# Kernel tuning notes

Measured on AMD Instinct MI355X. Metric: run time of the kernel, lower is better.

The kernel has to match this reference:

```python
import math
import jax
import jax.numpy as jnp
import numpy as np

B = 2; Hrv = 16; Wrv = 1024; Crv = 64; Cb = 128; Cout = 128
D = 128; K = 5; NH = 8; NP = 4; DH = D // NH
Hbev = 220; Wbev = 220
RMAX = 55.0; XMIN = -55.0; XMAX = 55.0; YMIN = -55.0; YMAX = 55.0
EDGE_GAIN = 4.0; KLW = 1e-4

ELEV = np.array([-30.67, -29.33, -28.0, -26.66, -25.33, -24.0, -22.67, -21.33, -20.0, -18.67, -17.33, -16.0, -14.67, -13.33, -12.0, -10.67, -9.33, -8.0, -6.66, -5.33, -4.0, -2.67, -1.33, 0.0, 1.33, 2.67, 4.0, 5.33, 6.67, 8.0, 9.33, 10.67], dtype=np.float32)


def _buffers():
    groups = ELEV[::-1].reshape(Hrv, 32 // Hrv)
    steps = np.deg2rad(groups.max(1) - groups.min(1)).astype(np.float32)
    # torch Tensor.repeat == tile (faithful to original, even though rows end up interleaved)
    elev_steps = np.tile(steps, Wrv).reshape(Hrv, Wrv)
    means = np.deg2rad(groups.mean(1)).astype(np.float32)
    elevation = np.repeat(means, Wrv).reshape(Hrv, Wrv)  # numpy repeat == elementwise
    az_line = np.linspace(-np.pi, np.pi, Wrv + 1, dtype=np.float64)[:-1]
    az_step = float(az_line[1] - az_line[0])
    az_line = (az_line + az_step / 2).astype(np.float32)
    azimuth = np.broadcast_to(az_line[None, :], (Hrv, Wrv)).astype(np.float32).copy()
    offsets = np.linspace(-0.6, 0.6, K).astype(np.float32)
    u_vec = np.stack([np.cos(elevation) * np.cos(azimuth), np.cos(elevation) * np.sin(azimuth), np.sin(elevation)], 0).astype(np.float32)
    return (jnp.asarray(elev_steps), jnp.asarray(elevation), jnp.asarray(azimuth), az_step, jnp.asarray(offsets), jnp.asarray(u_vec))


def conv1x1(x, w, b):
    return jnp.einsum('bchw,oc->bohw', x, w) + b[None, :, None, None]


def groupnorm(x, g, gamma, beta, eps=1e-5):
    b_, c, h, w = x.shape
    xr = x.reshape(b_, g, c // g, h, w)
    m = xr.mean(axis=(2, 3, 4), keepdims=True)
    v = xr.var(axis=(2, 3, 4), keepdims=True)
    xn = ((xr - m) * jax.lax.rsqrt(v + eps)).reshape(b_, c, h, w)
    return xn * gamma[None, :, None, None] + beta[None, :, None, None]


def bilinear_sample(v_t, loc, H, W):
    # v_t: [B,NH,H*W,DH]; loc: [B,Nq,NH,NP,2] in [0,1]; grid_sample align_corners=False, zeros pad
    x = loc[..., 0] * W - 0.5
    y = loc[..., 1] * H - 0.5
    x0 = jnp.floor(x); y0 = jnp.floor(y)
    wx = x - x0; wy = y - y0
    x0i = x0.astype(jnp.int32); y0i = y0.astype(jnp.int32)
    b_, n_, nh_, p_ = x.shape

    def gather(xi, yi):
        valid = (xi >= 0) & (xi < W) & (yi >= 0) & (yi < H)
        idx = jnp.clip(yi, 0, H - 1) * W + jnp.clip(xi, 0, W - 1)
        idx_t = idx.transpose(0, 2, 1, 3).reshape(b_, nh_, n_ * p_)
        g = jnp.take_along_axis(v_t, idx_t[..., None], axis=2).reshape(b_, nh_, n_, p_, -1)
        return g * valid.transpose(0, 2, 1, 3)[..., None]

    wxt = wx.transpose(0, 2, 1, 3)[..., None]
    wyt = wy.transpose(0, 2, 1, 3)[..., None]
    g = gather(x0i, y0i) * (1 - wxt) * (1 - wyt)
    g = g + gather(x0i + 1, y0i) * wxt * (1 - wyt)
    g = g + gather(x0i, y0i + 1) * (1 - wxt) * wyt
    g = g + gather(x0i + 1, y0i + 1) * wxt * wyt
    return g  # [B,NH,Nq,NP,DH]


def setup_inputs():
    key = jax.random.key(0)
    ks = jax.random.split(key, 20)
    def rn(k, shape, s=0.02):
        return jax.random.normal(k, shape, jnp.float32) * s
    inp = {}
    inp['x_rv'] = jax.random.normal(ks[0], (B, Hrv, Wrv, Crv), jnp.float32)
    inp['bev'] = jax.random.normal(ks[1], (B, Cb, Hbev, Wbev), jnp.float32)
    inp['lidar2ego_mat'] = jnp.eye(4, dtype=jnp.float32)[None] + 0.01 * jax.random.normal(ks[2], (1, 4, 4), jnp.float32)
    inp['w_q'] = rn(ks[3], (D, Crv)); inp['b_q'] = jnp.zeros((D,), jnp.float32)
    inp['w_v'] = rn(ks[4], (D, Cb)); inp['b_v'] = jnp.zeros((D,), jnp.float32)
    inp['w_o'] = rn(ks[5], (Cout, D)); inp['b_o'] = jnp.zeros((Cout,), jnp.float32)
    inp['qs_w1'] = rn(ks[6], (D, D + 6)); inp['qs_b1'] = jnp.zeros((D,), jnp.float32)
    inp['qs_w2'] = rn(ks[7], (D, D)); inp['qs_b2'] = jnp.zeros((D,), jnp.float32)
    inp['rh_w1'] = rn(ks[8], (128, Crv + 3)); inp['rh_b1'] = jnp.zeros((128,), jnp.float32)
    inp['rh_g1'] = jnp.ones((128,), jnp.float32); inp['rh_bt1'] = jnp.zeros((128,), jnp.float32)
    inp['rh_w2'] = rn(ks[9], (64, 128, 3, 3))
    inp['rh_g2'] = jnp.ones((64,), jnp.float32); inp['rh_bt2'] = jnp.zeros((64,), jnp.float32)
    inp['rh_w3'] = rn(ks[10], (4, 64)); inp['rh_b3'] = jnp.zeros((4,), jnp.float32)
    inp['off_w'] = rn(ks[11], (NH * K * NP * 2, D)); inp['off_b'] = rn(ks[12], (NH * K * NP * 2,), 0.5)
    inp['aw_w'] = rn(ks[13], (NH * K * NP, D)); inp['aw_b'] = jnp.zeros((NH * K * NP,), jnp.float32)
    inp['val_w'] = rn(ks[14], (D, D)); inp['val_b'] = jnp.zeros((D,), jnp.float32)
    inp['out_w'] = rn(ks[15], (D, D)); inp['out_b'] = jnp.zeros((D,), jnp.float32)
    return inp


def reference(x_rv, bev, lidar2ego_mat, w_q, b_q, w_v, b_v, w_o, b_o, qs_w1, qs_b1, qs_w2, qs_b2, rh_w1, rh_b1, rh_g1, rh_bt1, rh_w2, rh_g2, rh_bt2, rh_w3, rh_b3, off_w, off_b, aw_w, aw_b, val_w, val_b, out_w, out_b):
    elev_steps, elevation, azimuth, az_step, offsets, u_vec = _buffers()
    x = jnp.transpose(x_rv, (0, 3, 1, 2))  # [B,Crv,Hrv,Wrv]
    Q0 = conv1x1(x, w_q, b_q)
    Vmap = conv1x1(bev, w_v, b_v)
    range_in = jnp.concatenate([x, jnp.broadcast_to(u_vec[None], (B, 3, Hrv, Wrv))], axis=1)
    h = jax.nn.gelu(groupnorm(conv1x1(range_in, rh_w1, rh_b1), 8, rh_g1, rh_bt1), approximate=False)
    hp = jnp.pad(h, ((0, 0), (0, 0), (1, 1), (1, 1)), mode='wrap')  # circular padding
    h = jax.lax.conv_general_dilated(hp, rh_w2, (1, 1), 'VALID', dimension_numbers=('NCHW', 'OIHW', 'NCHW'))
    h = jax.nn.gelu(groupnorm(h, 8, rh_g2, rh_bt2), approximate=False)
    head = conv1x1(h, rh_w3, rh_b3)  # [B,4,Hrv,Wrv]
    mu = jax.nn.sigmoid(head[:, 0:1]) * RMAX
    sd = jax.nn.softplus(head[:, 1:2]) + 1e-3
    se = jax.nn.sigmoid(head[:, 2:3]) * elev_steps + 1e-3
    sa = jax.nn.sigmoid(head[:, 3:4]) * az_step + 1e-3
    depth = mu[:, 0][..., None] + sd[:, 0][..., None] * offsets  # [B,Hrv,Wrv,K]
    elevs = elevation[None, :, :, None] + se[:, 0][..., None] * offsets
    azs = azimuth[None, :, :, None] + sa[:, 0][..., None] * offsets
    ce = jnp.cos(elevs)
    x_l = depth * ce * jnp.cos(azs)
    y_l = depth * ce * jnp.sin(azs)
    z_l = depth * jnp.sin(elevs)
    NK = Hrv * Wrv * K
    p = jnp.stack([x_l.reshape(B, NK), y_l.reshape(B, NK), z_l.reshape(B, NK), jnp.ones((B, NK), x_l.dtype)], axis=-1)
    p_ego = jnp.matmul(p, lidar2ego_mat)  # [B,NK,4]
    rx = jax.nn.sigmoid(EDGE_GAIN * ((p_ego[..., 0] - XMIN) / (XMAX - XMIN) - 0.5))
    ry = jax.nn.sigmoid(EDGE_GAIN * ((p_ego[..., 1] - YMIN) / (YMAX - YMIN) - 0.5))
    ref = jnp.stack([rx, ry], axis=-1).reshape(B, Hrv * Wrv, K, 2)
    sig_feat = jnp.concatenate([sd, se, sa, 1.0 / (sd + 1e-6), 1.0 / (se + 1e-6), 1.0 / (sa + 1e-6)], axis=1)
    Q = conv1x1(jax.nn.gelu(conv1x1(jnp.concatenate([Q0, sig_feat], axis=1), qs_w1, qs_b1), approximate=False), qs_w2, qs_b2)
    query = jnp.transpose(Q, (0, 2, 3, 1)).reshape(B, Hrv * Wrv, D)
    value = jnp.transpose(Vmap.reshape(B, D, Hbev * Wbev), (0, 2, 1))  # [B,HW,D]
    # MSDA -- all K levels share the same BEV value map (value was repeat(1,K,1))
    v = (value @ val_w.T + val_b).reshape(B, Hbev * Wbev, NH, DH)
    v_t = jnp.transpose(v, (0, 2, 1, 3))  # [B,NH,HW,DH]
    Nq = Hrv * Wrv
    smp_off = (query @ off_w.T + off_b).reshape(B, Nq, NH, K, NP, 2)
    attn = jax.nn.softmax((query @ aw_w.T + aw_b).reshape(B, Nq, NH, K * NP), axis=-1).reshape(B, Nq, NH, K, NP)
    norm = jnp.array([Wbev, Hbev], jnp.float32)
    loc = ref[:, :, None, :, None, :] + smp_off / norm  # [B,Nq,NH,K,NP,2]
    out = jnp.zeros((B, Nq, NH, DH), jnp.float32)
    for l in range(K):
        smp = bilinear_sample(v_t, loc[:, :, :, l], Hbev, Wbev)
        out = out + jnp.einsum('bhnpd,bnhp->bnhd', smp, attn[:, :, :, l])
    y_msda = out.reshape(B, Nq, D) @ out_w.T + out_b + query  # mmcv identity residual
    y = jnp.transpose(y_msda.reshape(B, Hrv, Wrv, D), (0, 3, 1, 2))
    y = conv1x1(y, w_o, b_o)
    mu_norm = mu / RMAX
    sr = jnp.maximum(sd, 1e-6)
    saz = sa / az_step
    sel = se / elev_steps
    L_kl = 0.5 * (mu_norm ** 2 + sr ** 2 - jnp.log(sr ** 2) - 1.0) \
         + 0.5 * (saz ** 2 - jnp.log(saz ** 2) - 1.0) \
         + 0.5 * (sel ** 2 - jnp.log(sel ** 2) - 1.0)
    kl = KLW * L_kl.mean()
    y = y.reshape(B, Hrv, Wrv, -1)  # faithful to torch .view on NCHW (no permute)
    return (y, kl)
```

## Files before the change

### kernel.cpp

```cpp
#include <hip/hip_runtime.h>
#include <math.h>

#define HRV 16
#define WRV 1024
#define NPIX 16384
#define NBEV 48400
#define BSZ 2

typedef __attribute__((ext_vector_type(8))) short short8;
typedef __attribute__((ext_vector_type(4))) float f32x4;

struct RVConsts {
  float steps[16];
  float means[16];
  float az_step_f;
  float pad_;
  double step_d;
  double az0;
  double az_half;
};

__device__ __forceinline__ float geluf(float x) {
  return 0.5f * x * (1.0f + erff(x * 0.70710678118654752440f));
}
__device__ __forceinline__ float sigmoidf_(float x) {
  return 1.0f / (1.0f + expf(-x));
}
__device__ __forceinline__ float softplusf_(float x) {
  return fmaxf(x, 0.0f) + log1pf(expf(-fabsf(x)));
}
__device__ __forceinline__ float azimf(int w, double step_d, double az0, double az_half) {
  double az = (double)w * step_d + az0;
  az += az_half;
  return (float)az;
}
__device__ __forceinline__ unsigned short f2bf(float f) {
  unsigned int u = __builtin_bit_cast(unsigned int, f);
  u = u + 0x7FFFu + ((u >> 16) & 1u);
  return (unsigned short)(u >> 16);
}
__device__ __forceinline__ float bf2f(unsigned short h) {
  unsigned int u = ((unsigned int)h) << 16;
  return __builtin_bit_cast(float, u);
}

__global__ __launch_bounds__(256) void k_rh1_q0(
    const float* __restrict__ x_rv,
    const unsigned short* __restrict__ rhW1p, const float* __restrict__ rh_b1,
    const unsigned short* __restrict__ wqp, const float* __restrict__ b_q,
    float* __restrict__ t1, unsigned short* __restrict__ q0,
    float* __restrict__ sums1, RVConsts C) {
  __shared__ unsigned short xin[64][104];
  __shared__ float wred[4][8][2];
  int b = blockIdx.y;
  int n0 = blockIdx.x * 64;
  int tid = threadIdx.x;
  const float* src = x_rv + ((size_t)b * NPIX + n0) * 64;
  for (int i = tid; i < 1024; i += 256) {
    int p = i >> 4, c = (i & 15) * 4;
    float4 v4 = *(const float4*)(src + p * 64 + c);
    xin[p][c] = f2bf(v4.x);
    xin[p][c + 1] = f2bf(v4.y);
    xin[p][c + 2] = f2bf(v4.z);
    xin[p][c + 3] = f2bf(v4.w);
  }
  if (tid < 64) {
    int n = n0 + tid;
    int h = n >> 10, w = n & 1023;
    float E = C.means[h];
    float A = azimf(w, C.step_d, C.az0, C.az_half);
    float ce = cosf(E);
    xin[tid][64] = f2bf(ce * cosf(A));
    xin[tid][65] = f2bf(ce * sinf(A));
    xin[tid][66] = f2bf(sinf(E));
    for (int c = 67; c < 104; c++) xin[tid][c] = 0;
  }
  __syncthreads();
  int wave = tid >> 6, l = tid & 63;
  int lr = l & 15, lk = l >> 4;
  f32x4 acc[8], accq[8];
#pragma unroll
  for (int nt = 0; nt < 8; nt++) {
    float b1 = rh_b1[nt * 16 + lr], b2 = b_q[nt * 16 + lr];
    acc[nt] = (f32x4){b1, b1, b1, b1};
    accq[nt] = (f32x4){b2, b2, b2, b2};
  }
#pragma unroll
  for (int ks = 0; ks < 3; ks++) {
    short8 a = *(const short8*)&xin[wave * 16 + lr][ks * 32 + lk * 8];
#pragma unroll
    for (int nt = 0; nt < 8; nt++) {
      short8 b1v = *(const short8*)(rhW1p + (size_t)(nt * 16 + lr) * 96 + ks * 32 + lk * 8);
      acc[nt] = __builtin_amdgcn_mfma_f32_16x16x32_bf16(a, b1v, acc[nt], 0, 0, 0);
      short8 b2v = *(const short8*)(wqp + (size_t)(nt * 16 + lr) * 96 + ks * 32 + lk * 8);
      accq[nt] = __builtin_amdgcn_mfma_f32_16x16x32_bf16(a, b2v, accq[nt], 0, 0, 0);
    }
  }
#pragma unroll
  for (int nt = 0; nt < 8; nt++) {
    int n = nt * 16 + lr;
#pragma unroll
    for (int r = 0; r < 4; r++) {
      int p = n0 + wave * 16 + lk * 4 + r;
      size_t o = ((size_t)b * NPIX + p) * 128 + n;
      t1[o] = acc[nt][r];
      q0[o] = f2bf(accq[nt][r]);
    }
  }
  float s1[8], ss1[8];
#pragma unroll
  for (int nt = 0; nt < 8; nt++) {
    float a0 = acc[nt][0], a1 = acc[nt][1], a2 = acc[nt][2], a3 = acc[nt][3];
    s1[nt] = a0 + a1 + a2 + a3;
    ss1[nt] = a0 * a0 + a1 * a1 + a2 * a2 + a3 * a3;
  }
#pragma unroll
  for (int nt = 0; nt < 8; nt++) {
    s1[nt] += __shfl_xor(s1[nt], 1);  ss1[nt] += __shfl_xor(ss1[nt], 1);
    s1[nt] += __shfl_xor(s1[nt], 2);  ss1[nt] += __shfl_xor(ss1[nt], 2);
    s1[nt] += __shfl_xor(s1[nt], 4);  ss1[nt] += __shfl_xor(ss1[nt], 4);
    s1[nt] += __shfl_xor(s1[nt], 8);  ss1[nt] += __shfl_xor(ss1[nt], 8);
    s1[nt] += __shfl_xor(s1[nt], 16); ss1[nt] += __shfl_xor(ss1[nt], 16);
    s1[nt] += __shfl_xor(s1[nt], 32); ss1[nt] += __shfl_xor(ss1[nt], 32);
  }
  if (l == 0) {
#pragma unroll
    for (int nt = 0; nt < 8; nt++) { wred[wave][nt][0] = s1[nt]; wred[wave][nt][1] = ss1[nt]; }
  }
  __syncthreads();
  if (tid < 8) {
    float S = wred[0][tid][0] + wred[1][tid][0] + wred[2][tid][0] + wred[3][tid][0];
    float SS = wred[0][tid][1] + wred[1][tid][1] + wred[2][tid][1] + wred[3][tid][1];
    sums1[(((size_t)b * 8 + tid) * 256 + blockIdx.x) * 2 + 0] = S;
    sums1[(((size_t)b * 8 + tid) * 256 + blockIdx.x) * 2 + 1] = SS;
  }
}

__device__ __forceinline__ int cswz2(int row, int colw, int c) {
  int byte = ((row * 10 + colw) << 8) + (c << 1);
  return byte ^ ((row & 7) << 4);
}
__global__ __launch_bounds__(256) void k_conv3g(
    const float* __restrict__ t1, const float* __restrict__ sums1,
    const float* __restrict__ g1, const float* __restrict__ bt1,
    const unsigned short* __restrict__ w2p,
    float* __restrict__ t2, float* __restrict__ sums2) {
  __shared__ unsigned short tile[16 * 10 * 128];
  __shared__ float st[8][2];
  __shared__ float wred[4][2][4][2];
  int b = blockIdx.y;
  int w0 = blockIdx.x * 8;
  int tid = threadIdx.x;
  if (tid < 8) {
    int g = tid;
    float S = 0.f, SS = 0.f;
    for (int ch = 0; ch < 256; ch++) {
      S += sums1[(((size_t)b * 8 + g) * 256 + ch) * 2];
      SS += sums1[(((size_t)b * 8 + g) * 256 + ch) * 2 + 1];
    }
    float m = S * (1.0f / 262144.0f);
    float var = SS * (1.0f / 262144.0f) - m * m;
    st[g][0] = m;
    st[g][1] = rsqrtf(var + 1e-5f);
  }
  __syncthreads();
  for (int i = tid; i < 5120; i += 256) {
    int row = i / 320;
    int rem = i - row * 320;
    int colw = rem >> 5;
    int c4 = (rem & 31) * 4;
    int wc = (w0 + colw - 1 + WRV) & (WRV - 1);
    float4 x4 = *(const float4*)(t1 + ((size_t)b * NPIX + row * WRV + wc) * 128 + c4);
    int g = c4 >> 4;
    float m = st[g][0], is = st[g][1];
    float4 g4 = *(const float4*)(g1 + c4);
    float4 b4 = *(const float4*)(bt1 + c4);
    float y0 = geluf((x4.x - m) * is * g4.x + b4.x);
    float y1 = geluf((x4.y - m) * is * g4.y + b4.y);
    float y2 = geluf((x4.z - m) * is * g4.z + b4.z);
    float y3 = geluf((x4.w - m) * is * g4.w + b4.w);
    uint2 o;
    o.x = (unsigned int)f2bf(y0) | ((unsigned int)f2bf(y1) << 16);
    o.y = (unsigned int)f2bf(y2) | ((unsigned int)f2bf(y3) << 16);
    *(uint2*)((char*)tile + cswz2(row, colw, c4)) = o;
  }
  __syncthreads();
  int wave = tid >> 6, l = tid & 63;
  int lr = l & 15, lk = l >> 4;
  f32x4 acc[2][4];
#pragma unroll
  for (int cc2 = 0; cc2 < 2; cc2++)
#pragma unroll
    for (int nt = 0; nt < 4; nt++) acc[cc2][nt] = (f32x4){0.f, 0.f, 0.f, 0.f};
#pragma unroll
  for (int kpos = 0; kpos < 9; kpos++) {
    int ky = kpos / 3, kx = kpos - ky * 3;
    int arow = (lr + ky - 1 + 16) & 15;
#pragma unroll
    for (int cc2 = 0; cc2 < 2; cc2++) {
      int acol = wave * 2 + cc2 + kx;
#pragma unroll
      for (int ks = 0; ks < 4; ks++) {
        short8 a = *(const short8*)((const char*)tile + cswz2(arow, acol, ks * 32 + lk * 8));
#pragma unroll
        for (int nt = 0; nt < 4; nt++) {
          short8 bv = *(const short8*)(w2p + (size_t)(kpos * 64 + nt * 16 + lr) * 128 +
                                       ks * 32 + lk * 8);
          acc[cc2][nt] = __builtin_amdgcn_mfma_f32_16x16x32_bf16(a, bv, acc[cc2][nt], 0, 0, 0);
        }
      }
    }
  }
#pragma unroll
  for (int cc2 = 0; cc2 < 2; cc2++) {
    int cc = wave * 2 + cc2;
#pragma unroll
    for (int nt = 0; nt < 4; nt++) {
      int o = nt * 16 + lr;
#pragma unroll
      for (int r = 0; r < 4; r++) {
        int p = (lk * 4 + r) * WRV + w0 + cc;
        t2[((size_t)b * NPIX + p) * 64 + o] = acc[cc2][nt][r];
      }
    }
  }
  float ps[4], pss[4];
#pragma unroll
  for (int nt = 0; nt < 4; nt++) { ps[nt] = 0.f; pss[nt] = 0.f; }
#pragma unroll
  for (int cc2 = 0; cc2 < 2; cc2++)
#pragma unroll
    for (int nt = 0; nt < 4; nt++)
#pragma unroll
      for (int r = 0; r < 4; r++) {
        float v = acc[cc2][nt][r];
        ps[nt] += v;
        pss[nt] += v * v;
      }
#pragma unroll
  for (int nt = 0; nt < 4; nt++) {
    ps[nt] += __shfl_xor(ps[nt], 1);  pss[nt] += __shfl_xor(pss[nt], 1);
    ps[nt] += __shfl_xor(ps[nt], 2);  pss[nt] += __shfl_xor(pss[nt], 2);
    ps[nt] += __shfl_xor(ps[nt], 4);  pss[nt] += __shfl_xor(pss[nt], 4);
    ps[nt] += __shfl_xor(ps[nt], 16); pss[nt] += __shfl_xor(pss[nt], 16);
    ps[nt] += __shfl_xor(ps[nt], 32); pss[nt] += __shfl_xor(pss[nt], 32);
  }
  if ((l & 0x37) == 0) {
    int b3 = (l >> 3) & 1;
#pragma unroll
    for (int nt = 0; nt < 4; nt++) {
      wred[wave][b3][nt][0] = ps[nt];
      wred[wave][b3][nt][1] = pss[nt];
    }
  }
  __syncthreads();
  if (tid < 8) {
    int nt = tid >> 1, b3 = tid & 1;
    float S = 0.f, SS = 0.f;
    for (int wv = 0; wv < 4; wv++) { S += wred[wv][b3][nt][0]; SS += wred[wv][b3][nt][1]; }
    int g = nt * 2 + b3;
    sums2[(((size_t)b * 8 + g) * 128 + blockIdx.x) * 2 + 0] = S;
    sums2[(((size_t)b * 8 + g) * 128 + blockIdx.x) * 2 + 1] = SS;
  }
}

__global__ __launch_bounds__(256) void k_headquery(
    const float* __restrict__ t2, const float* __restrict__ sums2,
    const float* __restrict__ g2, const float* __restrict__ bt2,
    const float* __restrict__ rh_w3, const float* __restrict__ rh_b3,
    const float* __restrict__ l2e, const unsigned short* __restrict__ q0,
    const unsigned short* __restrict__ qsW1p, const float* __restrict__ qs_b1,
    const float* __restrict__ qs_w1f,
    const unsigned short* __restrict__ qsW2p, const float* __restrict__ qs_b2,
    float* __restrict__ params, float* __restrict__ klpart,
    unsigned short* __restrict__ query, RVConsts C) {
  __shared__ float st2[8][2];
  __shared__ unsigned short qin[64][136];
  __shared__ unsigned short hq[64][136];
  __shared__ float sigf[64][6];
  __shared__ float klred[64];
  int b = blockIdx.y;
  int n0 = blockIdx.x * 64;
  int tid = threadIdx.x;
  if (tid < 8) {
    int g = tid;
    float S = 0.f, SS = 0.f;
    for (int ch = 0; ch < 128; ch++) {
      S += sums2[(((size_t)b * 8 + g) * 128 + ch) * 2];
      SS += sums2[(((size_t)b * 8 + g) * 128 + ch) * 2 + 1];
    }
    float m = S * (1.0f / 131072.0f);
    float var = SS * (1.0f / 131072.0f) - m * m;
    st2[g][0] = m;
    st2[g][1] = rsqrtf(var + 1e-5f);
  }
  const unsigned short* src = q0 + ((size_t)b * NPIX + n0) * 128;
  for (int i = tid; i < 1024; i += 256) {
    int p = i >> 4, c0 = (i & 15) * 8;
    *(uint4*)&qin[p][c0] = *(const uint4*)(src + p * 128 + c0);
  }
  __syncthreads();
  {
    int px = tid >> 2, q = tid & 3;
    int n = n0 + px;
    int h = n >> 10, w = n & 1023;
    const float* t = t2 + ((size_t)b * NPIX + n) * 64 + q * 16;
    float hd0 = 0.f, hd1 = 0.f, hd2 = 0.f, hd3 = 0.f;
#pragma unroll
    for (int j = 0; j < 16; j++) {
      int c = q * 16 + j;
      int g = c >> 3;
      float xv = geluf((t[j] - st2[g][0]) * st2[g][1] * g2[c] + bt2[c]);
      hd0 += rh_w3[c] * xv;
      hd1 += rh_w3[64 + c] * xv;
      hd2 += rh_w3[128 + c] * xv;
      hd3 += rh_w3[192 + c] * xv;
    }
    hd0 += __shfl_xor(hd0, 1); hd1 += __shfl_xor(hd1, 1);
    hd2 += __shfl_xor(hd2, 1); hd3 += __shfl_xor(hd3, 1);
    hd0 += __shfl_xor(hd0, 2); hd1 += __shfl_xor(hd1, 2);
    hd2 += __shfl_xor(hd2, 2); hd3 += __shfl_xor(hd3, 2);
    if (q == 0) {
      hd0 += rh_b3[0]; hd1 += rh_b3[1]; hd2 += rh_b3[2]; hd3 += rh_b3[3];
      float mu = sigmoidf_(hd0) * 55.0f;
      float sd = softplusf_(hd1) + 1e-3f;
      float stepw = C.steps[w & 15];
      float se = sigmoidf_(hd2) * stepw + 1e-3f;
      float sa = sigmoidf_(hd3) * C.az_step_f + 1e-3f;
      float E0 = C.means[h];
      float A0 = azimf(w, C.step_d, C.az0, C.az_half);
      float* P = params + ((size_t)b * NPIX + n) * 16;
      P[0] = sd; P[1] = se; P[2] = sa;
      sigf[px][0] = sd; sigf[px][1] = se; sigf[px][2] = sa;
      sigf[px][3] = 1.0f / (sd + 1e-6f);
      sigf[px][4] = 1.0f / (se + 1e-6f);
      sigf[px][5] = 1.0f / (sa + 1e-6f);
      float M00 = l2e[0], M01 = l2e[1], M10 = l2e[4], M11 = l2e[5];
      float M20 = l2e[8], M21 = l2e[9], M30 = l2e[12], M31 = l2e[13];
#pragma unroll
      for (int k = 0; k < 5; k++) {
        float off = -0.6f + 0.3f * (float)k;
        float d = mu + sd * off;
        float E = E0 + se * off;
        float A = A0 + sa * off;
        float ce = cosf(E);
        float xl = d * ce * cosf(A), yl = d * ce * sinf(A), zl = d * sinf(E);
        float px_ = xl * M00 + yl * M10 + zl * M20 + M30;
        float py_ = xl * M01 + yl * M11 + zl * M21 + M31;
        P[3 + 2 * k] = sigmoidf_(4.0f * ((px_ + 55.0f) * (1.0f / 110.0f) - 0.5f));
        P[4 + 2 * k] = sigmoidf_(4.0f * ((py_ + 55.0f) * (1.0f / 110.0f) - 0.5f));
      }
      float mu_n = mu * (1.0f / 55.0f);
      float sr = fmaxf(sd, 1e-6f);
      float saz = sa / C.az_step_f;
      float sel = se / stepw;
      klred[px] = 0.5f * (mu_n * mu_n + sr * sr - logf(sr * sr) - 1.0f) +
                  0.5f * (saz * saz - logf(saz * saz) - 1.0f) +
                  0.5f * (sel * sel - logf(sel * sel) - 1.0f);
    }
  }
  __syncthreads();
  if (tid == 0) {
    float sL = 0.f;
    for (int i = 0; i < 64; i++) sL += klred[i];
    klpart[b * 256 + blockIdx.x] = sL;
  }
  int wave = tid >> 6, l = tid & 63;
  int lr = l & 15, lk = l >> 4;
  f32x4 acc[8];
#pragma unroll
  for (int nt = 0; nt < 8; nt++) {
    int n = nt * 16 + lr;
    float wt[6];
#pragma unroll
    for (int c = 0; c < 6; c++) wt[c] = qs_w1f[(size_t)n * 134 + 128 + c];
    float bias = qs_b1[n];
#pragma unroll
    for (int r = 0; r < 4; r++) {
      int pl = wave * 16 + lk * 4 + r;
      float a = bias;
#pragma unroll
      for (int c = 0; c < 6; c++) a += wt[c] * sigf[pl][c];
      acc[nt][r] = a;
    }
  }
#pragma unroll
  for (int ks = 0; ks < 4; ks++) {
    short8 a = *(const short8*)&qin[wave * 16 + lr][ks * 32 + lk * 8];
#pragma unroll
    for (int nt = 0; nt < 8; nt++) {
      short8 bv = *(const short8*)(qsW1p + (size_t)(nt * 16 + lr) * 128 + ks * 32 + lk * 8);
      acc[nt] = __builtin_amdgcn_mfma_f32_16x16x32_bf16(a, bv, acc[nt], 0, 0, 0);
    }
  }
#pragma unroll
  for (int nt = 0; nt < 8; nt++)
#pragma unroll
    for (int r = 0; r < 4; r++)
      hq[wave * 16 + lk * 4 + r][nt * 16 + lr] = f2bf(geluf(acc[nt][r]));
  __syncthreads();
#pragma unroll
  for (int nt = 0; nt < 8; nt++) {
    float bias = qs_b2[nt * 16 + lr];
    acc[nt] = (f32x4){bias, bias, bias, bias};
  }
#pragma unroll
  for (int ks = 0; ks < 4; ks++) {
    short8 a = *(const short8*)&hq[wave * 16 + lr][ks * 32 + lk * 8];
#pragma unroll
    for (int nt = 0; nt < 8; nt++) {
      short8 bv = *(const short8*)(qsW2p + (size_t)(nt * 16 + lr) * 128 + ks * 32 + lk * 8);
      acc[nt] = __builtin_amdgcn_mfma_f32_16x16x32_bf16(a, bv, acc[nt], 0, 0, 0);
    }
  }
#pragma unroll
  for (int nt = 0; nt < 8; nt++) {
    int n = nt * 16 + lr;
#pragma unroll
    for (int r = 0; r < 4; r++) {
      int p = n0 + wave * 16 + lk * 4 + r;
      query[((size_t)b * NPIX + p) * 128 + n] = f2bf(acc[nt][r]);
    }
  }
}

__global__ __launch_bounds__(256) void k_pack(
    const float* __restrict__ val_w, const float* __restrict__ w_v,
    const float* __restrict__ b_v, const float* __restrict__ val_b,
    const float* __restrict__ off_w, const float* __restrict__ off_b,
    const float* __restrict__ aw_w, const float* __restrict__ aw_b,
    const float* __restrict__ out_w, const float* __restrict__ qs_w1,
    const float* __restrict__ qs_w2, const float* __restrict__ rh_w1,
    const float* __restrict__ w_q, const float* __restrict__ w_o,
    const float* __restrict__ rh_w2,
    unsigned short* __restrict__ wvv_bf, float* __restrict__ bvv,
    unsigned short* __restrict__ projW, float* __restrict__ projB,
    unsigned short* __restrict__ outW, unsigned short* __restrict__ qsW1p,
    unsigned short* __restrict__ qsW2p, unsigned short* __restrict__ rhW1p,
    unsigned short* __restrict__ wqp, unsigned short* __restrict__ woP,
    unsigned short* __restrict__ w2p) {
  int idx = blockIdx.x * 256 + threadIdx.x;
  if (idx < 16384) {
    int o = idx >> 7, c = idx & 127;
    float acc = 0.0f;
    for (int m = 0; m < 128; m++) acc += val_w[o * 128 + m] * w_v[m * 128 + c];
    wvv_bf[idx] = f2bf(acc);
  } else if (idx < 16512) {
    int o = idx - 16384;
    float acc = val_b[o];
    for (int m = 0; m < 128; m++) acc += val_w[o * 128 + m] * b_v[m];
    bvv[o] = acc;
  } else if (idx < 82048) {
    int j = idx - 16512;
    int r = j >> 7, c = j & 127;
    float w = (r < 320) ? off_w[r * 128 + c] : ((r < 480) ? aw_w[(r - 320) * 128 + c] : 0.0f);
    projW[j] = f2bf(w);
  } else if (idx < 82560) {
    int r = idx - 82048;
    projB[r] = (r < 320) ? off_b[r] : ((r < 480) ? aw_b[r - 320] : 0.0f);
  } else if (idx < 98944) {
    int j = idx - 82560;
    outW[j] = f2bf(out_w[j]);
  } else if (idx < 115328) {
    int j = idx - 98944;
    int r = j >> 7, c = j & 127;
    qsW1p[j] = f2bf(qs_w1[r * 134 + c]);
  } else if (idx < 131712) {
    int j = idx - 115328;
    qsW2p[j] = f2bf(qs_w2[j]);
  } else if (idx < 144000) {
    int j = idx - 131712;
    int r = j / 96, c = j - r * 96;
    rhW1p[j] = (c < 67) ? f2bf(rh_w1[r * 67 + c]) : 0;
  } else if (idx < 156288) {
    int j = idx - 144000;
    int r = j / 96, c = j - r * 96;
    wqp[j] = (c < 64) ? f2bf(w_q[r * 64 + c]) : 0;
  } else if (idx < 172672) {
    int j = idx - 156288;
    woP[j] = f2bf(w_o[j]);
  } else if (idx < 246400) {
    int j = idx - 172672;
    int kpos = j >> 13;
    int rem = j & 8191;
    int o = rem >> 7, c = rem & 127;
    int ky = kpos / 3, kx = kpos - ky * 3;
    w2p[j] = f2bf(rh_w2[((size_t)(o * 128 + c) * 3 + ky) * 3 + kx]);
  }
}

__global__ __launch_bounds__(256) void k_value(
    const float* __restrict__ bev, const unsigned short* __restrict__ wvv_bf,
    const float* __restrict__ bvv, unsigned short* __restrict__ v) {
  __shared__ unsigned short lds[128 * 256];
  int b = blockIdx.y;
  int p0 = blockIdx.x * 256;
  int tid = threadIdx.x;
  for (int i = tid; i < 8192; i += 256) {
    int c = i >> 6;
    int p4 = (i & 63) * 4;
    int p = p0 + p4;
    float4 x;
    if (p + 3 < NBEV) {
      x = *(const float4*)(bev + ((size_t)b * 128 + c) * NBEV + p);
    } else {
      const float* row = bev + ((size_t)b * 128 + c) * NBEV;
      x.x = (p + 0 < NBEV) ? row[p + 0] : 0.0f;
      x.y = (p + 1 < NBEV) ? row[p + 1] : 0.0f;
      x.z = (p + 2 < NBEV) ? row[p + 2] : 0.0f;
      x.w = (p + 3 < NBEV) ? row[p + 3] : 0.0f;
    }
    uint2 o;
    o.x = (unsigned int)f2bf(x.x) | ((unsigned int)f2bf(x.y) << 16);
    o.y = (unsigned int)f2bf(x.z) | ((unsigned int)f2bf(x.w) << 16);
    int byte = (c << 9) + (p4 << 1);
    byte ^= ((c >> 3) & 7) << 4;
    *(uint2*)((char*)lds + byte) = o;
  }
  __syncthreads();
  int wave = tid >> 6, l = tid & 63;
  int lr = l & 15, lk = l >> 4;
#pragma unroll
  for (int sub = 0; sub < 4; sub++) {
    int ploc = sub * 64 + wave * 16 + lr;
    f32x4 acc[8];
#pragma unroll
    for (int nt = 0; nt < 8; nt++) {
      float bias = bvv[nt * 16 + lr];
      acc[nt] = (f32x4){bias, bias, bias, bias};
    }
#pragma unroll
    for (int ks = 0; ks < 4; ks++) {
      int k0 = ks * 32 + lk * 8;
      short8 a;
#pragma unroll
      for (int j = 0; j < 8; j++) {
        int k = k0 + j;
        int byte = (k << 9) + (ploc << 1);
        byte ^= ((k >> 3) & 7) << 4;
        a[j] = *(const short*)((const char*)lds + byte);
      }
#pragma unroll
      for (int nt = 0; nt < 8; nt++) {
        short8 bf = *(const short8*)(wvv_bf + (size_t)(nt * 16 + lr) * 128 + k0);
        acc[nt] = __builtin_amdgcn_mfma_f32_16x16x32_bf16(a, bf, acc[nt], 0, 0, 0);
      }
    }
#pragma unroll
    for (int nt = 0; nt < 8; nt++) {
      int n = nt * 16 + lr;
#pragma unroll
      for (int r = 0; r < 4; r++) {
        int p = p0 + sub * 64 + wave * 16 + lk * 4 + r;
        if (p < NBEV) v[((size_t)b * NBEV + p) * 128 + n] = f2bf(acc[nt][r]);
      }
    }
  }
}

__global__ __launch_bounds__(256) void k_proj(
    const unsigned short* __restrict__ query, const unsigned short* __restrict__ projW,
    const float* __restrict__ projB, unsigned short* __restrict__ proj) {
  __shared__ unsigned short qlds[64][136];
  int b = blockIdx.y;
  int p0b = blockIdx.x * 64;
  int tid = threadIdx.x;
  const unsigned short* src = query + ((size_t)b * NPIX + p0b) * 128;
  for (int i = tid; i < 1024; i += 256) {
    int p = i >> 4, c0 = (i & 15) * 8;
    *(uint4*)&qlds[p][c0] = *(const uint4*)(src + p * 128 + c0);
  }
  __syncthreads();
  int wave = tid >> 6, l = tid & 63;
  int lr = l & 15, lk = l >> 4;
  int p0 = p0b + wave * 16;
  for (int nc = 0; nc < 4; nc++) {
    int n0 = nc * 128;
    f32x4 acc[8];
#pragma unroll
    for (int nt = 0; nt < 8; nt++) {
      float bias = projB[n0 + nt * 16 + lr];
      acc[nt] = (f32x4){bias, bias, bias, bias};
    }
#pragma unroll
    for (int ks = 0; ks < 4; ks++) {
      short8 a = *(const short8*)&qlds[wave * 16 + lr][ks * 32 + lk * 8];
#pragma unroll
      for (int nt = 0; nt < 8; nt++) {
        short8 bf = *(const short8*)(projW + (size_t)(n0 + nt * 16 + lr) * 128 +
                                     ks * 32 + lk * 8);
        acc[nt] = __builtin_amdgcn_mfma_f32_16x16x32_bf16(a, bf, acc[nt], 0, 0, 0);
      }
    }
#pragma unroll
    for (int nt = 0; nt < 8; nt++) {
      int n = n0 + nt * 16 + lr;
#pragma unroll
      for (int r = 0; r < 4; r++) {
        int p = p0 + lk * 4 + r;
        proj[((size_t)b * NPIX + p) * 512 + n] = f2bf(acc[nt][r]);
      }
    }
  }
}

__global__ __launch_bounds__(256) void k_samp(
    const unsigned short* __restrict__ proj, const float* __restrict__ params,
    const unsigned short* __restrict__ v, unsigned short* __restrict__ S) {
  int b = blockIdx.y;
  int bid = blockIdx.x;
  int pb = (bid & 7) * 512 + (bid >> 3);
  int tid = threadIdx.x;
  int g = tid & 7;
  int hh = (tid >> 3) & 7;
  int pl = tid >> 6;
  int ts = g >> 1, th = g & 1;
  int n = pb * 4 + pl;
  const unsigned short* base = proj + ((size_t)b * NPIX + n) * 512;
  float lg[5];
#pragma unroll
  for (int t = 0; t < 5; t++) lg[t] = bf2f(base[320 + hh * 20 + ts * 5 + t]);
  float mx = fmaxf(fmaxf(fmaxf(lg[0], lg[1]), fmaxf(lg[2], lg[3])), lg[4]);
  mx = fmaxf(mx, __shfl_xor(mx, 2));
  mx = fmaxf(mx, __shfl_xor(mx, 4));
  float e[5];
  float s = 0.0f;
#pragma unroll
  for (int t = 0; t < 5; t++) { e[t] = expf(lg[t] - mx); s += e[t]; }
  s += __shfl_xor(s, 2);
  s += __shfl_xor(s, 4);
  float rs = 1.0f / s;
  const float* P = params + ((size_t)b * NPIX + n) * 16;
  const unsigned short* vb = v + (size_t)b * NBEV * 128 + hh * 16 + th * 8;
  float acc[8];
#pragma unroll
  for (int c = 0; c < 8; c++) acc[c] = 0.0f;
#pragma unroll
  for (int t = 0; t < 5; t++) {
    int kp = ts * 5 + t;
    int k = kp >> 2;
    unsigned int u = *(const unsigned int*)(base + hh * 40 + kp * 2);
    float X = P[3 + 2 * k] * 220.0f - 0.5f + bf2f((unsigned short)(u & 0xffffu));
    float Y = P[4 + 2 * k] * 220.0f - 0.5f + bf2f((unsigned short)(u >> 16));
    float xf = floorf(X), yf = floorf(Y);
    float wx = X - xf, wy = Y - yf;
    int x0 = (int)xf, y0 = (int)yf;
    float wx0 = ((unsigned)x0 < 220u) ? (1.0f - wx) : 0.0f;
    float wx1 = ((unsigned)(x0 + 1) < 220u) ? wx : 0.0f;
    float wy0 = ((unsigned)y0 < 220u) ? (1.0f - wy) : 0.0f;
    float wy1 = ((unsigned)(y0 + 1) < 220u) ? wy : 0.0f;
    int cx0 = min(max(x0, 0), 219), cx1 = min(max(x0 + 1, 0), 219);
    int cy0 = min(max(y0, 0), 219) * 220, cy1 = min(max(y0 + 1, 0), 219) * 220;
    float a = e[t] * rs;
    float u0 = a * wy0, u1 = a * wy1;
    float w4[4] = {u0 * wx0, u0 * wx1, u1 * wx0, u1 * wx1};
    int i4[4] = {cy0 + cx0, cy0 + cx1, cy1 + cx0, cy1 + cx1};
#pragma unroll
    for (int c2 = 0; c2 < 4; c2++) {
      float w = w4[c2];
      const uint2* sp = (const uint2*)(vb + (size_t)i4[c2] * 128);
      uint2 r0 = sp[0], r1 = sp[1];
      acc[0] += w * bf2f((unsigned short)(r0.x & 0xffffu));
      acc[1] += w * bf2f((unsigned short)(r0.x >> 16));
      acc[2] += w * bf2f((unsigned short)(r0.y & 0xffffu));
      acc[3] += w * bf2f((unsigned short)(r0.y >> 16));
      acc[4] += w * bf2f((unsigned short)(r1.x & 0xffffu));
      acc[5] += w * bf2f((unsigned short)(r1.x >> 16));
      acc[6] += w * bf2f((unsigned short)(r1.y & 0xffffu));
      acc[7] += w * bf2f((unsigned short)(r1.y >> 16));
    }
  }
#pragma unroll
  for (int c = 0; c < 8; c++) {
    acc[c] += __shfl_xor(acc[c], 2);
    acc[c] += __shfl_xor(acc[c], 4);
  }
  if (ts == 0) {
    uint4 o1;
    o1.x = (unsigned int)f2bf(acc[0]) | ((unsigned int)f2bf(acc[1]) << 16);
    o1.y = (unsigned int)f2bf(acc[2]) | ((unsigned int)f2bf(acc[3]) << 16);
    o1.z = (unsigned int)f2bf(acc[4]) | ((unsigned int)f2bf(acc[5]) << 16);
    o1.w = (unsigned int)f2bf(acc[6]) | ((unsigned int)f2bf(acc[7]) << 16);
    *(uint4*)(S + ((size_t)b * NPIX + n) * 128 + hh * 16 + th * 8) = o1;
  }
}

__global__ __launch_bounds__(256) void k_outfinal(
    const unsigned short* __restrict__ S, const unsigned short* __restrict__ outW,
    const float* __restrict__ out_b, const unsigned short* __restrict__ query,
    const unsigned short* __restrict__ woP, const float* __restrict__ b_o,
    const float* __restrict__ klpart, float* __restrict__ out) {
  __shared__ unsigned short ylds[64][136];
  __shared__ float yt[128][67];
  int b = blockIdx.y;
  int p0b = blockIdx.x * 64;
  int tid = threadIdx.x;
  int wave = tid >> 6, l = tid & 63;
  int lr = l & 15, lk = l >> 4;
  {
    f32x4 acc[8];
#pragma unroll
    for (int nt = 0; nt < 8; nt++) {
      float bias = out_b[nt * 16 + lr];
      acc[nt] = (f32x4){bias, bias, bias, bias};
    }
    const unsigned short* ap = S + ((size_t)b * NPIX + p0b + wave * 16 + lr) * 128 + lk * 8;
#pragma unroll
    for (int ks = 0; ks < 4; ks++) {
      short8 a = *(const short8*)(ap + ks * 32);
#pragma unroll
      for (int nt = 0; nt < 8; nt++) {
        short8 bf = *(const short8*)(outW + (size_t)(nt * 16 + lr) * 128 + ks * 32 + lk * 8);
        acc[nt] = __builtin_amdgcn_mfma_f32_16x16x32_bf16(a, bf, acc[nt], 0, 0, 0);
      }
    }
#pragma unroll
    for (int nt = 0; nt < 8; nt++) {
      int n = nt * 16 + lr;
#pragma unroll
      for (int r = 0; r < 4; r++) {
        int p_local = wave * 16 + lk * 4 + r;
        size_t o = ((size_t)b * NPIX + p0b + p_local) * 128 + n;
        ylds[p_local][n] = f2bf(acc[nt][r] + bf2f(query[o]));
      }
    }
  }
  __syncthreads();
  {
    f32x4 acc[8];
#pragma unroll
    for (int nt = 0; nt < 8; nt++) {
      float bias = b_o[nt * 16 + lr];
      acc[nt] = (f32x4){bias, bias, bias, bias};
    }
#pragma unroll
    for (int ks = 0; ks < 4; ks++) {
      short8 a = *(const short8*)&ylds[wave * 16 + lr][ks * 32 + lk * 8];
#pragma unroll
      for (int nt = 0; nt < 8; nt++) {
        short8 bf = *(const short8*)(woP + (size_t)(nt * 16 + lr) * 128 + ks * 32 + lk * 8);
        acc[nt] = __builtin_amdgcn_mfma_f32_16x16x32_bf16(a, bf, acc[nt], 0, 0, 0);
      }
    }
#pragma unroll
    for (int nt = 0; nt < 8; nt++)
#pragma unroll
      for (int r = 0; r < 4; r++)
        yt[nt * 16 + lr][wave * 16 + lk * 4 + r] = acc[nt][r];
  }
  __syncthreads();
  int n = tid >> 1, half = tid & 1;
  float* dst = out + ((size_t)(b * 128 + n)) * NPIX + p0b + half * 32;
#pragma unroll
  for (int j = 0; j < 8; j++) {
    float4 v4 = {yt[n][half * 32 + j * 4], yt[n][half * 32 + j * 4 + 1],
                 yt[n][half * 32 + j * 4 + 2], yt[n][half * 32 + j * 4 + 3]};
    *(float4*)(dst + j * 4) = v4;
  }
  if (blockIdx.x == 0 && b == 0 && tid == 0) {
    float sL = 0.0f;
    for (int i = 0; i < 512; i++) sL += klpart[i];
    out[(size_t)BSZ * 128 * NPIX] = 1e-4f * (sL / 32768.0f);
  }
}

static RVConsts make_consts() {
  static const float ELEV[32] = {
      -30.67f, -29.33f, -28.0f, -26.66f, -25.33f, -24.0f, -22.67f, -21.33f,
      -20.0f,  -18.67f, -17.33f, -16.0f, -14.67f, -13.33f, -12.0f, -10.67f,
      -9.33f,  -8.0f,   -6.66f,  -5.33f, -4.0f,   -2.67f,  -1.33f, 0.0f,
      1.33f,   2.67f,   4.0f,    5.33f,  6.67f,   8.0f,    9.33f,  10.67f};
  RVConsts C;
  const float d2r = 0.017453292519943295f;
  for (int r = 0; r < 16; r++) {
    float a = ELEV[31 - 2 * r], b = ELEV[30 - 2 * r];
    float mx = fmaxf(a, b), mn = fminf(a, b);
    C.steps[r] = (mx - mn) * d2r;
    C.means[r] = ((a + b) * 0.5f) * d2r;
  }
  const double PI_D = 3.14159265358979323846;
  double step_d = (PI_D - (-PI_D)) / 1024.0;
  double az0 = -PI_D;
  double az1 = az0 + step_d;
  double az_step_d = az1 - az0;
  C.az_step_f = (float)az_step_d;
  C.pad_ = 0.0f;
  C.step_d = step_d;
  C.az0 = az0;
  C.az_half = az_step_d * 0.5;
  return C;
}

#define OFF_T1     0u
#define OFF_T2     8388608u
#define OFF_Q0     10485760u
#define OFF_PARAMS 14680064u
#define OFF_QUERY  15204352u
#define OFF_S      19398656u
#define OFF_SUMS1  21495808u
#define OFF_SUMS2  21504000u
#define OFF_KL     21508096u
#define OFF_PROJ   0u
#define OFF_V      8388608u
#define OFF_WVV    21508608u
#define OFF_BVV    21516800u
#define OFF_PROJW  21516928u
#define OFF_PROJB  21549696u
#define OFF_OUTW   21550208u
#define OFF_QSW1   21558400u
#define OFF_QSW2   21566592u
#define OFF_RHW1   21574784u
#define OFF_WQP    21580928u
#define OFF_WOP    21587072u
#define OFF_W2P    21595264u

extern "C" void kernel_launch(void* const* d_in, const int* in_sizes, int n_in,
                              void* d_out, int out_size, void* d_ws, size_t ws_size,
                              hipStream_t stream) {
  const float* x_rv = (const float*)d_in[0];
  const float* bev = (const float*)d_in[1];
  const float* l2e = (const float*)d_in[2];
  const float* w_q = (const float*)d_in[3];
  const float* b_q = (const float*)d_in[4];
  const float* w_v = (const float*)d_in[5];
  const float* b_v = (const float*)d_in[6];
  const float* w_o = (const float*)d_in[7];
  const float* b_o = (const float*)d_in[8];
  const float* qs_w1 = (const float*)d_in[9];
  const float* qs_b1 = (const float*)d_in[10];
  const float* qs_w2 = (const float*)d_in[11];
  const float* qs_b2 = (const float*)d_in[12];
  const float* rh_w1 = (const float*)d_in[13];
  const float* rh_b1 = (const float*)d_in[14];
  const float* rh_g1 = (const float*)d_in[15];
  const float* rh_bt1 = (const float*)d_in[16];
  const float* rh_w2 = (const float*)d_in[17];
  const float* rh_g2 = (const float*)d_in[18];
  const float* rh_bt2 = (const float*)d_in[19];
  const float* rh_w3 = (const float*)d_in[20];
  const float* rh_b3 = (const float*)d_in[21];
  const float* off_w = (const float*)d_in[22];
  const float* off_b = (const float*)d_in[23];
  const float* aw_w = (const float*)d_in[24];
  const float* aw_b = (const float*)d_in[25];
  const float* val_w = (const float*)d_in[26];
  const float* val_b = (const float*)d_in[27];
  const float* out_w = (const float*)d_in[28];
  const float* out_b = (const float*)d_in[29];

  float* ws = (float*)d_ws;
  float* t1 = ws + OFF_T1;
  float* t2 = ws + OFF_T2;
  float* params = ws + OFF_PARAMS;
  float* sums1 = ws + OFF_SUMS1;
  float* sums2 = ws + OFF_SUMS2;
  float* klpart = ws + OFF_KL;
  float* bvv = ws + OFF_BVV;
  float* projB = ws + OFF_PROJB;
  unsigned short* q0bf = (unsigned short*)(ws + OFF_Q0);
  unsigned short* querybf = (unsigned short*)(ws + OFF_QUERY);
  unsigned short* S_bf = (unsigned short*)(ws + OFF_S);
  unsigned short* proj_bf = (unsigned short*)(ws + OFF_PROJ);
  unsigned short* v_bf = (unsigned short*)(ws + OFF_V);
  unsigned short* wvv_bf = (unsigned short*)(ws + OFF_WVV);
  unsigned short* projW = (unsigned short*)(ws + OFF_PROJW);
  unsigned short* outW = (unsigned short*)(ws + OFF_OUTW);
  unsigned short* qsW1p = (unsigned short*)(ws + OFF_QSW1);
  unsigned short* qsW2p = (unsigned short*)(ws + OFF_QSW2);
  unsigned short* rhW1p = (unsigned short*)(ws + OFF_RHW1);
  unsigned short* wqp = (unsigned short*)(ws + OFF_WQP);
  unsigned short* woP = (unsigned short*)(ws + OFF_WOP);
  unsigned short* w2p = (unsigned short*)(ws + OFF_W2P);

  RVConsts C = make_consts();
  dim3 blk(256);

  k_pack<<<963, blk, 0, stream>>>(val_w, w_v, b_v, val_b, off_w, off_b, aw_w, aw_b, out_w,
                                  qs_w1, qs_w2, rh_w1, w_q, w_o, rh_w2,
                                  wvv_bf, bvv, projW, projB, outW, qsW1p, qsW2p, rhW1p,
                                  wqp, woP, w2p);
  k_rh1_q0<<<dim3(256, BSZ), blk, 0, stream>>>(x_rv, rhW1p, rh_b1, wqp, b_q, t1, q0bf,
                                               sums1, C);
  k_conv3g<<<dim3(128, BSZ), blk, 0, stream>>>(t1, sums1, rh_g1, rh_bt1, w2p, t2, sums2);
  k_headquery<<<dim3(256, BSZ), blk, 0, stream>>>(t2, sums2, rh_g2, rh_bt2, rh_w3, rh_b3,
                                                  l2e, q0bf, qsW1p, qs_b1, qs_w1, qsW2p,
                                                  qs_b2, params, klpart, querybf, C);
  k_value<<<dim3(190, BSZ), blk, 0, stream>>>(bev, wvv_bf, bvv, v_bf);
  k_proj<<<dim3(256, BSZ), blk, 0, stream>>>(querybf, projW, projB, proj_bf);
  k_samp<<<dim3(4096, BSZ), blk, 0, stream>>>(proj_bf, params, v_bf, S_bf);
  k_outfinal<<<dim3(256, BSZ), blk, 0, stream>>>(S_bf, outW, out_b, querybf, woP, b_o,
                                                 klpart, (float*)d_out);
}
```

Baseline: 270.8 us.

## Restructure value projection LDS layout and stage outputs for coalesced stores

The value-projection kernel now transposes BEV input into a pixel-major swizzled LDS tile, so each MFMA A-fragment is one 16-byte LDS load instead of eight scalar loads. Results go through a second swizzled LDS buffer and are written to global memory as coalesced 16-byte stores, replacing scattered 2-byte stores. The block tile shrinks from 256 to 128 pixels and the grid doubles, which adds parallelism and cuts LDS per block. The cost is scalar 2-byte LDS writes during the transpose and two extra barriers per sub-tile.

```diff
diff --git a/kernel.cpp b/kernel.cpp
--- a/kernel.cpp
+++ b/kernel.cpp
@@ -489,16 +489,25 @@
   }
 }
 
+__device__ __forceinline__ int aswz(int p, int k) {
+  int byte = (p << 8) + (k << 1);
+  return byte ^ (((((p >> 2) ^ p)) & 15) << 4);
+}
+__device__ __forceinline__ int vswz(int pl, int n) {
+  int byte = (pl << 8) + (n << 1);
+  return byte ^ ((pl & 15) << 4);
+}
 __global__ __launch_bounds__(256) void k_value(
     const float* __restrict__ bev, const unsigned short* __restrict__ wvv_bf,
     const float* __restrict__ bvv, unsigned short* __restrict__ v) {
-  __shared__ unsigned short lds[128 * 256];
+  __shared__ unsigned short ash[128 * 128];
+  __shared__ unsigned short vout[64 * 128];
   int b = blockIdx.y;
-  int p0 = blockIdx.x * 256;
+  int p0 = blockIdx.x * 128;
   int tid = threadIdx.x;
-  for (int i = tid; i < 8192; i += 256) {
-    int c = i >> 6;
-    int p4 = (i & 63) * 4;
+  for (int i = tid; i < 4096; i += 256) {
+    int c = i >> 5;
+    int p4 = (i & 31) * 4;
     int p = p0 + p4;
     float4 x;
     if (p + 3 < NBEV) {
@@ -510,19 +519,18 @@
       x.z = (p + 2 < NBEV) ? row[p + 2] : 0.0f;
       x.w = (p + 3 < NBEV) ? row[p + 3] : 0.0f;
     }
-    uint2 o;
-    o.x = (unsigned int)f2bf(x.x) | ((unsigned int)f2bf(x.y) << 16);
-    o.y = (unsigned int)f2bf(x.z) | ((unsigned int)f2bf(x.w) << 16);
-    int byte = (c << 9) + (p4 << 1);
-    byte ^= ((c >> 3) & 7) << 4;
-    *(uint2*)((char*)lds + byte) = o;
+    unsigned short hv0 = f2bf(x.x), hv1 = f2bf(x.y), hv2 = f2bf(x.z), hv3 = f2bf(x.w);
+    *(unsigned short*)((char*)ash + aswz(p4 + 0, c)) = hv0;
+    *(unsigned short*)((char*)ash + aswz(p4 + 1, c)) = hv1;
+    *(unsigned short*)((char*)ash + aswz(p4 + 2, c)) = hv2;
+    *(unsigned short*)((char*)ash + aswz(p4 + 3, c)) = hv3;
   }
   __syncthreads();
   int wave = tid >> 6, l = tid & 63;
   int lr = l & 15, lk = l >> 4;
-#pragma unroll
-  for (int sub = 0; sub < 4; sub++) {
-    int ploc = sub * 64 + wave * 16 + lr;
+  for (int sub = 0; sub < 2; sub++) {
+    int plb = sub * 64;
+    int ploc = plb + wave * 16 + lr;
     f32x4 acc[8];
 #pragma unroll
     for (int nt = 0; nt < 8; nt++) {
@@ -532,14 +540,7 @@
 #pragma unroll
     for (int ks = 0; ks < 4; ks++) {
       int k0 = ks * 32 + lk * 8;
-      short8 a;
-#pragma unroll
-      for (int j = 0; j < 8; j++) {
-        int k = k0 + j;
-        int byte = (k << 9) + (ploc << 1);
-        byte ^= ((k >> 3) & 7) << 4;
-        a[j] = *(const short*)((const char*)lds + byte);
-      }
+      short8 a = *(const short8*)((const char*)ash + aswz(ploc, k0));
 #pragma unroll
       for (int nt = 0; nt < 8; nt++) {
         short8 bf = *(const short8*)(wvv_bf + (size_t)(nt * 16 + lr) * 128 + k0);
@@ -551,10 +552,21 @@
       int n = nt * 16 + lr;
 #pragma unroll
       for (int r = 0; r < 4; r++) {
-        int p = p0 + sub * 64 + wave * 16 + lk * 4 + r;
-        if (p < NBEV) v[((size_t)b * NBEV + p) * 128 + n] = f2bf(acc[nt][r]);
-      }
-    }
+        int pl = wave * 16 + lk * 4 + r;
+        *(unsigned short*)((char*)vout + vswz(pl, n)) = f2bf(acc[nt][r]);
+      }
+    }
+    __syncthreads();
+#pragma unroll
+    for (int j = 0; j < 4; j++) {
+      int idx = tid + j * 256;
+      int pl = idx >> 4;
+      int ns = (idx & 15) * 8;
+      uint4 val = *(const uint4*)((const char*)vout + vswz(pl, ns));
+      int p = p0 + plb + pl;
+      if (p < NBEV) *(uint4*)(v + ((size_t)b * NBEV + p) * 128 + ns) = val;
+    }
+    __syncthreads();
   }
 }
 
@@ -885,7 +897,7 @@
   k_headquery<<<dim3(256, BSZ), blk, 0, stream>>>(t2, sums2, rh_g2, rh_bt2, rh_w3, rh_b3,
                                                   l2e, q0bf, qsW1p, qs_b1, qs_w1, qsW2p,
                                                   qs_b2, params, klpart, querybf, C);
-  k_value<<<dim3(190, BSZ), blk, 0, stream>>>(bev, wvv_bf, bvv, v_bf);
+  k_value<<<dim3(379, BSZ), blk, 0, stream>>>(bev, wvv_bf, bvv, v_bf);
   k_proj<<<dim3(256, BSZ), blk, 0, stream>>>(querybf, projW, projB, proj_bf);
   k_samp<<<dim3(4096, BSZ), blk, 0, stream>>>(proj_bf, params, v_bf, S_bf);
   k_outfinal<<<dim3(256, BSZ), blk, 0, stream>>>(S_bf, outW, out_b, querybf, woP, b_o,
```

After: 257.5 us. 4.9% less time.
